# Kernel tuning notes

Measured on AMD Instinct MI355X. Metric: run time of the kernel, lower is better.

## Reference

```python
import jax, jax.numpy as jnp
import numpy as np

B, CIR_LEN, AUX_DIM, T, CD, DS, DCONV = 16, 16384, 14, 512, 256, 16, 4
SEG = CIR_LEN // T          # 32
DI = 2 * CD                 # d_inner = 512


def layer_norm(x, g, b, eps=1e-5):
    m = jnp.mean(x, -1, keepdims=True)
    v = jnp.var(x, -1, keepdims=True)
    return (x - m) * jax.lax.rsqrt(v + eps) * g + b


def gelu(x):
    return jax.nn.gelu(x, approximate=False)  # torch default exact GELU


def selective_ssm(x, in_proj_w, conv_w, conv_b, x_proj_w, dt_proj_w, dt_proj_b, A_log, D, out_proj_w):
    # x: (B, L, CD)
    Bsz, L, _ = x.shape
    xz = x @ in_proj_w.T                      # (B, L, 2*DI)
    x_in, z = jnp.split(xz, 2, axis=-1)       # each (B, L, DI)
    # depthwise causal conv (pad d_conv-1 left, truncate to L == torch pad both + [:L])
    xp = jnp.pad(x_in, ((0, 0), (DCONV - 1, 0), (0, 0)))
    x_conv = sum(xp[:, k:k + L, :] * conv_w[:, k] for k in range(DCONV)) + conv_b
    x_conv = jax.nn.silu(x_conv)              # (B, L, DI)
    ssm_in = x_conv @ x_proj_w.T              # (B, L, 1+2*DS)
    dt_raw = ssm_in[..., :1]
    B_ssm = ssm_in[..., 1:1 + DS]             # (B, L, DS)
    C_ssm = ssm_in[..., 1 + DS:]              # (B, L, DS)
    delta = jax.nn.softplus(dt_raw @ dt_proj_w.T + dt_proj_b)      # (B, L, DI)
    A = -jnp.exp(A_log)                                            # (DI, DS)
    deltaA = jnp.exp(delta[..., None] * A)                         # (B, L, DI, DS)
    deltaB_u = delta[..., None] * B_ssm[:, :, None, :] * x_conv[..., None]

    def step(h, inp):
        dA, dBu, c = inp
        h = dA * h + dBu                       # (B, DI, DS)
        y = jnp.einsum('bds,bs->bd', h, c)     # (B, DI)
        return h, y

    h0 = jnp.zeros((Bsz, DI, DS), x.dtype)
    _, ys = jax.lax.scan(step, h0, (jnp.moveaxis(deltaA, 1, 0),
                                    jnp.moveaxis(deltaB_u, 1, 0),
                                    jnp.moveaxis(C_ssm, 1, 0)))
    y = jnp.moveaxis(ys, 0, 1)                 # (B, L, DI)
    y = y + x_conv * D
    y = y * jax.nn.silu(z)
    return y @ out_proj_w.T                    # (B, L, CD)


def setup_inputs() -> dict:
    key = jax.random.key(0)
    ks = iter(jax.random.split(key, 32))
    rn = lambda shape, s=0.02: jax.random.normal(next(ks), shape, jnp.float32) * s
    return {
        'cir': jax.random.normal(next(ks), (B, CIR_LEN), jnp.float32),
        'aux': jax.random.normal(next(ks), (B, AUX_DIM), jnp.float32),
        'cir_proj_w': rn((CD, SEG)),
        'cir_norm_g': jnp.ones((CD,)), 'cir_norm_b': jnp.zeros((CD,)),
        'aux_proj_w': rn((CD, AUX_DIM)),
        'aux_norm_g': jnp.ones((CD,)), 'aux_norm_b': jnp.zeros((CD,)),
        'm_norm_g': jnp.ones((CD,)), 'm_norm_b': jnp.zeros((CD,)),
        'in_proj_w': rn((2 * DI, CD)),
        'conv_w': rn((DI, DCONV)), 'conv_b': jnp.zeros((DI,)),
        'x_proj_w': rn((1 + 2 * DS, DI)),
        'dt_proj_w': rn((DI, 1)), 'dt_proj_b': jnp.zeros((DI,)),
        'A_log': jnp.log(jnp.broadcast_to(jnp.arange(1, DS + 1, dtype=jnp.float32), (DI, DS))),
        'D': jnp.ones((DI,)),
        'out_proj_w': rn((CD, DI)),
        'mid_w': rn((CD, CD)), 'mid_b': jnp.zeros((CD,)),
        'mid_norm_g': jnp.ones((CD,)), 'mid_norm_b': jnp.zeros((CD,)),
        'bn_g': jnp.ones((CD,)), 'bn_b': jnp.zeros((CD,)),
        'fc1_w': rn((CD // 2, CD)), 'fc1_b': jnp.zeros((CD // 2,)),
        'fc2_w': rn((1, CD // 2)), 'fc2_b': jnp.zeros((1,)),
    }


def reference(cir, aux, cir_proj_w, cir_norm_g, cir_norm_b, aux_proj_w, aux_norm_g, aux_norm_b,
              m_norm_g, m_norm_b, in_proj_w, conv_w, conv_b, x_proj_w, dt_proj_w, dt_proj_b,
              A_log, D, out_proj_w, mid_w, mid_b, mid_norm_g, mid_norm_b, bn_g, bn_b,
              fc1_w, fc1_b, fc2_w, fc2_b):
    # eval mode: dropout = identity, BatchNorm uses running stats (mean 0, var 1)
    x_seg = cir.reshape(cir.shape[0], T, SEG)
    h_cir = gelu(layer_norm(x_seg @ cir_proj_w.T, cir_norm_g, cir_norm_b))
    h_aux = gelu(layer_norm(aux @ aux_proj_w.T, aux_norm_g, aux_norm_b))[:, None, :]
    h = h_cir + h_aux                          # (B, T, CD)
    h = h + selective_ssm(layer_norm(h, m_norm_g, m_norm_b), in_proj_w, conv_w, conv_b,
                          x_proj_w, dt_proj_w, dt_proj_b, A_log, D, out_proj_w)
    hp = jnp.mean(h, axis=1)                   # AdaptiveAvgPool1d(1)
    h2 = gelu(layer_norm(hp @ mid_w.T + mid_b, mid_norm_g, mid_norm_b))
    hbn = h2 * jax.lax.rsqrt(jnp.float32(1.0 + 1e-5)) * bn_g + bn_b
    h3 = gelu(hbn @ fc1_w.T + fc1_b)
    return (h3 @ fc2_w.T + fc2_b)[:, 0]
```

## Files before the change

kernel.cpp:

```cpp
#include <hip/hip_runtime.h>
#include <hip/hip_bf16.h>

typedef __hip_bfloat16 bf16;
typedef __attribute__((ext_vector_type(8))) short short8;
typedef __attribute__((ext_vector_type(4))) float f32x4;

#define Bsz   16
#define Tn    512
#define SEG   32
#define CD    256
#define DI    512
#define DS    16
#define DCONV 4
#define BT    (Bsz*Tn)
#define NPART 32

__device__ __forceinline__ float erf_fast(float x) {
  float ax = fabsf(x);
  float t = 1.0f / (1.0f + 0.3275911f * ax);
  float p = t * (0.254829592f + t * (-0.284496736f + t * (1.421413741f +
            t * (-1.453152027f + t * 1.061405429f))));
  float r = 1.0f - p * __expf(-ax * ax);
  return copysignf(r, x);
}
__device__ __forceinline__ float gelu_f(float x) {
  return 0.5f * x * (1.0f + erf_fast(x * 0.7071067811865476f));
}
__device__ __forceinline__ float silu_f(float x) {
  return x / (1.0f + __expf(-x));
}
__device__ __forceinline__ float softplus_f(float x) {
  return fmaxf(x, 0.0f) + __logf(1.0f + __expf(-fabsf(x)));
}
__device__ __forceinline__ float bfu(unsigned short u) {
  return __uint_as_float(((unsigned int)u) << 16);
}
__device__ __forceinline__ unsigned short f2bfu(float x) {
  bf16 h = __float2bfloat16(x);
  return *(unsigned short*)&h;
}
__device__ __forceinline__ float block_sum256(float v, float* red) {
  int tid = threadIdx.x;
  #pragma unroll
  for (int off = 32; off > 0; off >>= 1) v += __shfl_down(v, off, 64);
  __syncthreads();
  if ((tid & 63) == 0) red[tid >> 6] = v;
  __syncthreads();
  return red[0] + red[1] + red[2] + red[3];
}

__global__ __launch_bounds__(256) void prep_kernel(
    const float* __restrict__ aux, const float* __restrict__ apw,
    const float* __restrict__ g, const float* __restrict__ bb,
    const float* __restrict__ in_w, const float* __restrict__ xpw,
    const float* __restrict__ cpw,
    bf16* __restrict__ w_in, bf16* __restrict__ wpad, bf16* __restrict__ cpwT,
    float* __restrict__ haux)
{
  __shared__ float red[4];
  int i = blockIdx.x * 256 + threadIdx.x;
  if (i < 262144) {
    int e = i & 7, lane = (i >> 3) & 63, k0 = (i >> 9) & 7, nb = i >> 12;
    int fr = lane & 15, q = lane >> 4;
    w_in[i] = __float2bfloat16(in_w[(size_t)(nb * 16 + fr) * 256 + k0 * 32 + q * 8 + e]);
  } else if (i < 294912) {
    int o = i - 262144;
    int e = o & 7, lane = (o >> 3) & 63, k0 = (o >> 9) & 15, nb = o >> 13;
    int fr = lane & 15, q = lane >> 4;
    int row = nb * 16 + fr, k = k0 * 32 + q * 8 + e;
    float v = 0.f;
    if (row < 32)       v = xpw[(1 + row) * 512 + k];
    else if (row == 32) v = xpw[k];
    wpad[o] = __float2bfloat16(v);
  } else {
    int o = i - 294912;
    int k = o >> 8, j = o & 255;
    cpwT[o] = __float2bfloat16(cpw[j * 32 + k]);
  }
  if (blockIdx.x < 16) {
    int b = blockIdx.x, j = threadIdx.x;
    float acc = 0.f;
    #pragma unroll
    for (int k = 0; k < 14; ++k)
      acc += aux[b * 14 + k] * apw[j * 14 + k];
    float s1 = block_sum256(acc, red);
    float s2 = block_sum256(acc * acc, red);
    float mean = s1 * (1.f / 256.f);
    float var  = s2 * (1.f / 256.f) - mean * mean;
    float xn = (acc - mean) * rsqrtf(var + 1e-5f) * g[j] + bb[j];
    haux[b * 256 + j] = gelu_f(xn);
  }
}

__global__ __launch_bounds__(512) void row_inproj_kernel(
    const float* __restrict__ cir, const bf16* __restrict__ cpwT,
    const float* __restrict__ cg, const float* __restrict__ cb,
    const float* __restrict__ mg, const float* __restrict__ mb,
    const float* __restrict__ haux, const bf16* __restrict__ w_in,
    bf16* __restrict__ xzbf, float* __restrict__ hp_part)
{
  __shared__ float hps[8][256];
  __shared__ __align__(16) unsigned short xns[16][264];
  int tid = threadIdx.x;
  int wave = tid >> 6, lane = tid & 63;
  int r0 = blockIdx.x * 16 + wave * 2;
  int b = blockIdx.x >> 5;
  int j0 = lane * 4;

  float vj[2][4] = {};
  for (int c = 0; c < 8; ++c) {
    float xk[2][4];
    #pragma unroll
    for (int r4 = 0; r4 < 2; ++r4) {
      float4 xv = ((const float4*)(cir + (size_t)(r0 + r4) * SEG))[c];
      xk[r4][0] = xv.x; xk[r4][1] = xv.y; xk[r4][2] = xv.z; xk[r4][3] = xv.w;
    }
    #pragma unroll
    for (int kk = 0; kk < 4; ++kk) {
      int k = c * 4 + kk;
      uint2 wv = *(const uint2*)((const unsigned short*)cpwT + k * 256 + j0);
      float w0 = __uint_as_float(wv.x << 16);
      float w1 = __uint_as_float(wv.x & 0xffff0000u);
      float w2 = __uint_as_float(wv.y << 16);
      float w3 = __uint_as_float(wv.y & 0xffff0000u);
      #pragma unroll
      for (int r4 = 0; r4 < 2; ++r4) {
        float xv = xk[r4][kk];
        vj[r4][0] += xv * w0; vj[r4][1] += xv * w1;
        vj[r4][2] += xv * w2; vj[r4][3] += xv * w3;
      }
    }
  }
  float s[2], q2[2];
  #pragma unroll
  for (int r4 = 0; r4 < 2; ++r4) {
    s[r4]  = vj[r4][0] + vj[r4][1] + vj[r4][2] + vj[r4][3];
    q2[r4] = vj[r4][0]*vj[r4][0] + vj[r4][1]*vj[r4][1]
           + vj[r4][2]*vj[r4][2] + vj[r4][3]*vj[r4][3];
  }
  #pragma unroll
  for (int off = 32; off > 0; off >>= 1) {
    #pragma unroll
    for (int r4 = 0; r4 < 2; ++r4) {
      s[r4]  += __shfl_xor(s[r4],  off, 64);
      q2[r4] += __shfl_xor(q2[r4], off, 64);
    }
  }
  float4 cgv = *(const float4*)(cg + j0);
  float4 cbv = *(const float4*)(cb + j0);
  float4 hxv = *(const float4*)(haux + b * 256 + j0);
  float hv[2][4];
  float hs[2], hq[2];
  #pragma unroll
  for (int r4 = 0; r4 < 2; ++r4) {
    float mean = s[r4] * (1.f/256.f);
    float var  = q2[r4] * (1.f/256.f) - mean * mean;
    float inv  = rsqrtf(var + 1e-5f);
    float g0 = gelu_f((vj[r4][0] - mean) * inv * cgv.x + cbv.x) + hxv.x;
    float g1 = gelu_f((vj[r4][1] - mean) * inv * cgv.y + cbv.y) + hxv.y;
    float g2 = gelu_f((vj[r4][2] - mean) * inv * cgv.z + cbv.z) + hxv.z;
    float g3 = gelu_f((vj[r4][3] - mean) * inv * cgv.w + cbv.w) + hxv.w;
    hv[r4][0] = g0; hv[r4][1] = g1; hv[r4][2] = g2; hv[r4][3] = g3;
    hs[r4] = g0 + g1 + g2 + g3;
    hq[r4] = g0*g0 + g1*g1 + g2*g2 + g3*g3;
  }
  #pragma unroll
  for (int off = 32; off > 0; off >>= 1) {
    #pragma unroll
    for (int r4 = 0; r4 < 2; ++r4) {
      hs[r4] += __shfl_xor(hs[r4], off, 64);
      hq[r4] += __shfl_xor(hq[r4], off, 64);
    }
  }
  float4 mgv = *(const float4*)(mg + j0);
  float4 mbv = *(const float4*)(mb + j0);
  #pragma unroll
  for (int r4 = 0; r4 < 2; ++r4) {
    float m2  = hs[r4] * (1.f/256.f);
    float v2  = hq[r4] * (1.f/256.f) - m2 * m2;
    float inv2 = rsqrtf(v2 + 1e-5f);
    unsigned int lo = (unsigned int)f2bfu((hv[r4][0] - m2) * inv2 * mgv.x + mbv.x) |
                      ((unsigned int)f2bfu((hv[r4][1] - m2) * inv2 * mgv.y + mbv.y) << 16);
    unsigned int hi = (unsigned int)f2bfu((hv[r4][2] - m2) * inv2 * mgv.z + mbv.z) |
                      ((unsigned int)f2bfu((hv[r4][3] - m2) * inv2 * mgv.w + mbv.w) << 16);
    uint2 pk; pk.x = lo; pk.y = hi;
    *(uint2*)&xns[wave * 2 + r4][j0] = pk;
  }
  #pragma unroll
  for (int q = 0; q < 4; ++q)
    hps[wave][j0 + q] = hv[0][q] + hv[1][q];
  __syncthreads();
  if (tid < 256) {
    int j = tid;
    float part = hps[0][j] + hps[1][j] + hps[2][j] + hps[3][j]
               + hps[4][j] + hps[5][j] + hps[6][j] + hps[7][j];
    hp_part[(size_t)(blockIdx.x & (NPART - 1)) * 4096 + b * 256 + j] =
        part * (1.f / 512.f);
  }
  {
    int fr = lane & 15, quad = lane >> 4;
    int rbase = blockIdx.x * 16;
    const short* Wp = (const short*)w_in;
    unsigned short* xzp = (unsigned short*)xzbf;
    #pragma unroll
    for (int nt = 0; nt < 8; ++nt) {
      int nb = wave * 8 + nt;
      f32x4 acc = {0.f, 0.f, 0.f, 0.f};
      #pragma unroll
      for (int k0 = 0; k0 < 8; ++k0) {
        int ka = k0 * 32 + quad * 8;
        short8 a = *(const short8*)&xns[fr][ka];
        short8 bb8 = *(const short8*)(Wp + (((size_t)nb * 8 + k0) * 64 + lane) * 8);
        acc = __builtin_amdgcn_mfma_f32_16x16x32_bf16(a, bb8, acc, 0, 0, 0);
      }
      int n0 = nb * 16;
      int crow = quad * 4;
      #pragma unroll
      for (int i = 0; i < 4; ++i)
        xzp[(size_t)(rbase + crow + i) * 1024 + n0 + fr] = f2bfu(acc[i]);
    }
  }
}

__global__ __launch_bounds__(512) void conv_xproj_kernel(
    const bf16* __restrict__ xzbf, const bf16* __restrict__ wpad,
    const float* __restrict__ cw, const float* __restrict__ cbv,
    float* __restrict__ ssm)
{
  __shared__ __align__(16) unsigned short xst[35][512];
  __shared__ __align__(16) unsigned short xcs[32][520];
  int c = blockIdx.x, b = blockIdx.y;
  int t0 = c * 32;
  int tid = threadIdx.x;
  const unsigned short* xzp = (const unsigned short*)xzbf;

  for (int it = tid; it < 2240; it += 512) {
    int row = it >> 6, c8 = it & 63;
    int t = t0 - 3 + row;
    uint4 v = make_uint4(0u, 0u, 0u, 0u);
    if (t >= 0)
      v = *(const uint4*)(xzp + ((size_t)((b << 9) + t)) * 1024 + c8 * 8);
    *(uint4*)&xst[row][c8 * 8] = v;
  }
  __syncthreads();

  {
    int d = tid;
    float4 w = *(const float4*)(cw + d * 4);
    float cbd = cbv[d];
    float pa = bfu(xst[0][d]), pb = bfu(xst[1][d]), pc = bfu(xst[2][d]);
    #pragma unroll
    for (int i = 0; i < 32; ++i) {
      float x = bfu(xst[3 + i][d]);
      float a = cbd + w.x * pa + w.y * pb + w.z * pc + w.w * x;
      pa = pb; pb = pc; pc = x;
      xcs[i][d] = f2bfu(silu_f(a));
    }
  }
  __syncthreads();

  {
    int wave = tid >> 6, lane = tid & 63;
    int fr = lane & 15, quad = lane >> 4;
    int mh = wave >> 2;
    int nb = wave & 3;
    int n0 = nb * 16;
    f32x4 acc = {0.f, 0.f, 0.f, 0.f};
    const short* Wp = (const short*)wpad;
    #pragma unroll
    for (int k0 = 0; k0 < 16; ++k0) {
      int ka = k0 * 32 + quad * 8;
      short8 a = *(const short8*)&xcs[mh * 16 + fr][ka];
      short8 b8 = *(const short8*)(Wp + (((size_t)nb * 16 + k0) * 64 + lane) * 8);
      acc = __builtin_amdgcn_mfma_f32_16x16x32_bf16(a, b8, acc, 0, 0, 0);
    }
    int ccol = lane & 15, crow = quad * 4;
    #pragma unroll
    for (int i = 0; i < 4; ++i)
      ssm[((size_t)((b << 9) + t0 + mh * 16 + crow + i)) * 64 + n0 + ccol] = acc[i];
  }
}

__global__ __launch_bounds__(1024) void scan_full_kernel(
    const bf16* __restrict__ xzbf, const float* __restrict__ ssm,
    const float* __restrict__ cw, const float* __restrict__ cbv,
    const float* __restrict__ dtw, const float* __restrict__ dtb,
    const float* __restrict__ A_log, const float* __restrict__ Dd,
    float* __restrict__ ybar)
{
  __shared__ __align__(16) unsigned short xraw[2][35][32];
  __shared__ __align__(16) unsigned short zraw[2][32][32];
  __shared__ __align__(8)  float BC[2][32][34];
  __shared__ float dts[2][32];
  __shared__ __align__(16) float cgd[2][32][32][4];
  __shared__ float xdp_s[32][32];
  __shared__ float hendA[32][16];
  __shared__ float ybh[2][32];

  int dgrp = blockIdx.x, b = blockIdx.y;
  int tid = threadIdx.x;
  int d0 = dgrp * 32;
  int bb = b << 9;
  const unsigned short* xzp = (const unsigned short*)xzbf;

  int s  = tid & 15;
  int dp = (tid >> 4) & 31;
  int qh = tid >> 9;
  int dS = d0 + dp;
  float As  = -__expf(A_log[dS * 16 + s]);
  int d2 = tid & 31, r32 = (tid >> 5) & 31;
  int dC = d0 + d2;
  float4 wc = *(const float4*)(cw + dC * 4);
  float cbd = cbv[dC];
  float wdC = dtw[dC], bdC = dtb[dC];

  float h = 0.f, yacc = 0.f, P = 1.f, K = 0.f, xdp = 0.f;

  for (int p = 0; p < 8; ++p) {
    __syncthreads();
    if (tid < 512) {
      for (int it = tid; it < 536; it += 512) {
        int q = it >= 268;
        int e = it - (q ? 268 : 0);
        int t0q = q * 256 + p * 32;
        if (e < 140) {
          int row = e >> 2, c4 = e & 3;
          int t = t0q - 3 + row;
          uint4 v = make_uint4(0u, 0u, 0u, 0u);
          if (t >= 0)
            v = *(const uint4*)(xzp + (size_t)(bb + t) * 1024 + d0 + c4 * 8);
          *(uint4*)&xraw[q][row][c4 * 8] = v;
        } else {
          int e2 = e - 140;
          int row = e2 >> 2, c4 = e2 & 3;
          uint4 v = *(const uint4*)(xzp + (size_t)(bb + t0q + row) * 1024 + 512 + d0 + c4 * 8);
          *(uint4*)&zraw[q][row][c4 * 8] = v;
        }
      }
    } else {
      int t2 = tid - 512;
      int q = t2 >> 8;
      int r = (t2 >> 3) & 31, l8 = t2 & 7;
      int t0q = q * 256 + p * 32;
      const float* srow = ssm + (size_t)(bb + t0q + r) * 64;
      float4 v = *(const float4*)(srow + l8 * 4);
      int cc = l8 * 4;
      if (cc < 16) {
        BC[q][r][cc*2]   = v.x; BC[q][r][cc*2+2] = v.y;
        BC[q][r][cc*2+4] = v.z; BC[q][r][cc*2+6] = v.w;
      } else {
        int c2 = cc - 16;
        BC[q][r][c2*2+1] = v.x; BC[q][r][c2*2+3] = v.y;
        BC[q][r][c2*2+5] = v.z; BC[q][r][c2*2+7] = v.w;
      }
      if (l8 == 0) dts[q][r] = srow[32];
    }
    __syncthreads();
    #pragma unroll
    for (int q = 0; q < 2; ++q) {
      int ii = r32;
      float xa = bfu(xraw[q][ii][d2]);
      float xb = bfu(xraw[q][ii + 1][d2]);
      float xm = bfu(xraw[q][ii + 2][d2]);
      float xd = bfu(xraw[q][ii + 3][d2]);
      float a = cbd + wc.x * xa + wc.y * xb + wc.z * xm + wc.w * xd;
      float xc = bfu(f2bfu(silu_f(a)));
      float gt = silu_f(bfu(zraw[q][ii][d2]));
      float de = softplus_f(dts[q][ii] * wdC + bdC);
      xdp += xc * gt;
      float4 pk; pk.x = de * xc; pk.y = gt; pk.z = de; pk.w = 0.f;
      *(float4*)&cgd[q][ii][d2][0] = pk;
    }
    __syncthreads();
    #pragma unroll
    for (int i = 0; i < 32; ++i) {
      float4 cg = *(const float4*)&cgd[qh][i][dp][0];
      float2 bc = *(const float2*)&BC[qh][i][s * 2];
      float a = __expf(As * cg.z);
      h = a * h + cg.x * bc.x;
      float w = bc.y * cg.y;
      yacc += h * w;
      if (qh) { P *= a; K += P * w; }
    }
  }
  xdp_s[r32][d2] = xdp;
  if (qh == 0) hendA[dp][s] = h;
  __syncthreads();
  if (qh == 1) yacc += hendA[dp][s] * K;
  yacc += __shfl_xor(yacc, 1, 64);
  yacc += __shfl_xor(yacc, 2, 64);
  yacc += __shfl_xor(yacc, 4, 64);
  yacc += __shfl_xor(yacc, 8, 64);
  if (s == 0) ybh[qh][dp] = yacc;
  __syncthreads();
  if (qh == 0 && s == 0) {
    float xds = 0.f;
    #pragma unroll
    for (int k = 0; k < 32; ++k) xds += xdp_s[k][dp];
    ybar[b * 512 + dS] = ybh[0][dp] + ybh[1][dp] + Dd[dS] * xds;
  }
}

__global__ __launch_bounds__(256) void head_kernel(
    const float* __restrict__ hp_part, const float* __restrict__ ybar,
    const float* __restrict__ w_out,
    const float* __restrict__ midw, const float* __restrict__ midb,
    const float* __restrict__ mng, const float* __restrict__ mnb,
    const float* __restrict__ bng, const float* __restrict__ bnb,
    const float* __restrict__ f1w, const float* __restrict__ f1b,
    const float* __restrict__ f2w, const float* __restrict__ f2b,
    float* __restrict__ out)
{
  __shared__ float red[4];
  __shared__ __align__(16) float yb[512];
  __shared__ __align__(16) float shp[256];
  __shared__ __align__(16) float sh[256];
  __shared__ __align__(16) float sh2[128];
  int b = blockIdx.x, j = threadIdx.x;
  yb[j]       = ybar[b * 512 + j];
  yb[256 + j] = ybar[b * 512 + 256 + j];
  float hv = 0.f;
  #pragma unroll
  for (int p = 0; p < NPART; ++p)
    hv += hp_part[(size_t)p * 4096 + b * 256 + j];
  __syncthreads();
  {
    float acc2 = 0.f;
    const float4* wr = (const float4*)(w_out + j * 512);
    const float4* yv = (const float4*)yb;
    #pragma unroll 4
    for (int k = 0; k < 128; ++k) {
      float4 w = wr[k], x = yv[k];
      acc2 += w.x * x.x + w.y * x.y + w.z * x.z + w.w * x.w;
    }
    hv += acc2 * (1.f / 512.f);
  }
  shp[j] = hv;
  __syncthreads();
  float acc = midb[j];
  {
    const float4* mw = (const float4*)(midw + j * 256);
    const float4* sv = (const float4*)shp;
    #pragma unroll 4
    for (int k = 0; k < 64; ++k) {
      float4 w = mw[k], xv = sv[k];
      acc += w.x * xv.x + w.y * xv.y + w.z * xv.z + w.w * xv.w;
    }
  }
  float s1 = block_sum256(acc, red);
  float s2 = block_sum256(acc * acc, red);
  float mean = s1 * (1.f / 256.f);
  float var  = s2 * (1.f / 256.f) - mean * mean;
  float h2 = gelu_f((acc - mean) * rsqrtf(var + 1e-5f) * mng[j] + mnb[j]);
  float hbn = h2 * rsqrtf(1.0f + 1e-5f) * bng[j] + bnb[j];
  sh[j] = hbn;
  __syncthreads();
  if (j < 128) {
    float a2 = f1b[j];
    const float4* fw = (const float4*)(f1w + j * 256);
    const float4* sv = (const float4*)sh;
    #pragma unroll 4
    for (int k = 0; k < 64; ++k) {
      float4 w = fw[k], xv = sv[k];
      a2 += w.x * xv.x + w.y * xv.y + w.z * xv.z + w.w * xv.w;
    }
    sh2[j] = gelu_f(a2);
  }
  __syncthreads();
  if (j == 0) {
    float o = f2b[0];
    const float4* fw = (const float4*)f2w;
    const float4* sv = (const float4*)sh2;
    for (int k = 0; k < 32; ++k) {
      float4 w = fw[k], xv = sv[k];
      o += w.x * xv.x + w.y * xv.y + w.z * xv.z + w.w * xv.w;
    }
    out[b] = o;
  }
}

extern "C" void kernel_launch(void* const* d_in, const int* in_sizes, int n_in,
                              void* d_out, int out_size, void* d_ws, size_t ws_size,
                              hipStream_t stream)
{
  const float* cir        = (const float*)d_in[0];
  const float* aux        = (const float*)d_in[1];
  const float* cir_proj_w = (const float*)d_in[2];
  const float* cir_norm_g = (const float*)d_in[3];
  const float* cir_norm_b = (const float*)d_in[4];
  const float* aux_proj_w = (const float*)d_in[5];
  const float* aux_norm_g = (const float*)d_in[6];
  const float* aux_norm_b = (const float*)d_in[7];
  const float* m_norm_g   = (const float*)d_in[8];
  const float* m_norm_b   = (const float*)d_in[9];
  const float* in_proj_w  = (const float*)d_in[10];
  const float* conv_w     = (const float*)d_in[11];
  const float* conv_b     = (const float*)d_in[12];
  const float* x_proj_w   = (const float*)d_in[13];
  const float* dt_proj_w  = (const float*)d_in[14];
  const float* dt_proj_b  = (const float*)d_in[15];
  const float* A_log      = (const float*)d_in[16];
  const float* Dd         = (const float*)d_in[17];
  const float* out_proj_w = (const float*)d_in[18];
  const float* mid_w      = (const float*)d_in[19];
  const float* mid_b      = (const float*)d_in[20];
  const float* mid_norm_g = (const float*)d_in[21];
  const float* mid_norm_b = (const float*)d_in[22];
  const float* bn_g       = (const float*)d_in[23];
  const float* bn_b       = (const float*)d_in[24];
  const float* fc1_w      = (const float*)d_in[25];
  const float* fc1_b      = (const float*)d_in[26];
  const float* fc2_w      = (const float*)d_in[27];
  const float* fc2_b      = (const float*)d_in[28];
  float* out = (float*)d_out;

  float* ws      = (float*)d_ws;
  bf16*  xzbf    = (bf16*)ws;
  float* ssm     = ws + 4194304;
  bf16*  w_inbf  = (bf16*)(ssm + 524288);
  bf16*  wpadbf  = (bf16*)((float*)w_inbf + 131072);
  bf16*  cpwTbf  = (bf16*)((float*)wpadbf + 16384);
  float* haux    = (float*)cpwTbf + 4096;
  float* hp_part = haux + 4096;
  float* ybar    = hp_part + 131072;

  prep_kernel<<<1184, 256, 0, stream>>>(aux, aux_proj_w, aux_norm_g, aux_norm_b,
                                        in_proj_w, x_proj_w, cir_proj_w,
                                        w_inbf, wpadbf, cpwTbf, haux);
  row_inproj_kernel<<<512, 512, 0, stream>>>(cir, cpwTbf, cir_norm_g, cir_norm_b,
                                             m_norm_g, m_norm_b, haux, w_inbf,
                                             xzbf, hp_part);
  conv_xproj_kernel<<<dim3(16, Bsz), 512, 0, stream>>>(xzbf, wpadbf, conv_w, conv_b,
                                                       ssm);
  scan_full_kernel<<<dim3(16, Bsz), 1024, 0, stream>>>(xzbf, ssm, conv_w, conv_b,
                                                       dt_proj_w, dt_proj_b,
                                                       A_log, Dd, ybar);
  head_kernel<<<16, 256, 0, stream>>>(hp_part, ybar, out_proj_w,
                                      mid_w, mid_b, mid_norm_g, mid_norm_b,
                                      bn_g, bn_b, fc1_w, fc1_b, fc2_w, fc2_b, out);
}
```

Baseline: 215.0 us.

## Store z and conv output in per-channel-group transposed layout; reuse conv result in scan

The in-projection now writes x and z to separate buffers, with z laid out per batch and 32-channel group so each time step is a contiguous 64-byte row. The conv kernel also writes its SiLU conv output in the same transposed layout, so the scan reads ready conv values instead of recomputing the depthwise conv and SiLU. This removes redundant conv math and the strided 64-byte gathers from 2KB-stride rows in the scan's loads. The cost is an extra global write of the conv output and scattered 2-byte stores for z in the in-projection epilogue.

Measured after the change: 217.6 us. No clear change (+1.2%).

```diff
diff --git a/kernel.cpp b/kernel.cpp
--- a/kernel.cpp
+++ b/kernel.cpp
@@ -97,7 +97,8 @@
     const float* __restrict__ cg, const float* __restrict__ cb,
     const float* __restrict__ mg, const float* __restrict__ mb,
     const float* __restrict__ haux, const bf16* __restrict__ w_in,
-    bf16* __restrict__ xzbf, float* __restrict__ hp_part)
+    bf16* __restrict__ xbf, bf16* __restrict__ zTg,
+    float* __restrict__ hp_part)
 {
   __shared__ float hps[8][256];
   __shared__ __align__(16) unsigned short xns[16][264];
@@ -200,8 +201,10 @@
   {
     int fr = lane & 15, quad = lane >> 4;
     int rbase = blockIdx.x * 16;
+    int tl0 = (blockIdx.x & 31) * 16 + quad * 4;
     const short* Wp = (const short*)w_in;
-    unsigned short* xzp = (unsigned short*)xzbf;
+    unsigned short* xp = (unsigned short*)xbf;
+    unsigned short* zp = (unsigned short*)zTg;
     #pragma unroll
     for (int nt = 0; nt < 8; ++nt) {
       int nb = wave * 8 + nt;
@@ -213,33 +216,41 @@
         short8 bb8 = *(const short8*)(Wp + (((size_t)nb * 8 + k0) * 64 + lane) * 8);
         acc = __builtin_amdgcn_mfma_f32_16x16x32_bf16(a, bb8, acc, 0, 0, 0);
       }
-      int n0 = nb * 16;
+      int n = nb * 16 + fr;
       int crow = quad * 4;
-      #pragma unroll
-      for (int i = 0; i < 4; ++i)
-        xzp[(size_t)(rbase + crow + i) * 1024 + n0 + fr] = f2bfu(acc[i]);
+      if (nb < 32) {
+        #pragma unroll
+        for (int i = 0; i < 4; ++i)
+          xp[(size_t)(rbase + crow + i) * 512 + n] = f2bfu(acc[i]);
+      } else {
+        int d = n - 512, dg = d >> 5, d2 = d & 31;
+        size_t base = ((size_t)(b * 16 + dg) * 512 + tl0) * 32 + d2;
+        #pragma unroll
+        for (int i = 0; i < 4; ++i)
+          zp[base + (size_t)i * 32] = f2bfu(acc[i]);
+      }
     }
   }
 }
 
 __global__ __launch_bounds__(512) void conv_xproj_kernel(
-    const bf16* __restrict__ xzbf, const bf16* __restrict__ wpad,
+    const bf16* __restrict__ xbf, const bf16* __restrict__ wpad,
     const float* __restrict__ cw, const float* __restrict__ cbv,
-    float* __restrict__ ssm)
+    float* __restrict__ ssm, bf16* __restrict__ xcT)
 {
   __shared__ __align__(16) unsigned short xst[35][512];
   __shared__ __align__(16) unsigned short xcs[32][520];
   int c = blockIdx.x, b = blockIdx.y;
   int t0 = c * 32;
   int tid = threadIdx.x;
-  const unsigned short* xzp = (const unsigned short*)xzbf;
+  const unsigned short* xzp = (const unsigned short*)xbf;
 
   for (int it = tid; it < 2240; it += 512) {
     int row = it >> 6, c8 = it & 63;
     int t = t0 - 3 + row;
     uint4 v = make_uint4(0u, 0u, 0u, 0u);
     if (t >= 0)
-      v = *(const uint4*)(xzp + ((size_t)((b << 9) + t)) * 1024 + c8 * 8);
+      v = *(const uint4*)(xzp + ((size_t)((b << 9) + t)) * 512 + c8 * 8);
     *(uint4*)&xst[row][c8 * 8] = v;
   }
   __syncthreads();
@@ -258,6 +269,14 @@
     }
   }
   __syncthreads();
+
+  {
+    int dg = tid >> 5, tl = tid & 31;
+    uint4* dst = (uint4*)((unsigned short*)xcT +
+                          (((size_t)(b * 16 + dg)) * 512 + t0 + tl) * 32);
+    const uint4* src = (const uint4*)&xcs[tl][dg * 32];
+    dst[0] = src[0]; dst[1] = src[1]; dst[2] = src[2]; dst[3] = src[3];
+  }
 
   {
     int wave = tid >> 6, lane = tid & 63;
@@ -282,14 +301,14 @@
 }
 
 __global__ __launch_bounds__(1024) void scan_full_kernel(
-    const bf16* __restrict__ xzbf, const float* __restrict__ ssm,
-    const float* __restrict__ cw, const float* __restrict__ cbv,
+    const bf16* __restrict__ xcT, const bf16* __restrict__ zTg,
+    const float* __restrict__ ssm,
     const float* __restrict__ dtw, const float* __restrict__ dtb,
     const float* __restrict__ A_log, const float* __restrict__ Dd,
     float* __restrict__ ybar)
 {
-  __shared__ __align__(16) unsigned short xraw[2][35][32];
-  __shared__ __align__(16) unsigned short zraw[2][32][32];
+  __shared__ __align__(16) unsigned short xct[2][32][32];
+  __shared__ __align__(16) unsigned short zt[2][32][32];
   __shared__ __align__(8)  float BC[2][32][34];
   __shared__ float dts[2][32];
   __shared__ __align__(16) float cgd[2][32][32][4];
@@ -299,19 +318,16 @@
 
   int dgrp = blockIdx.x, b = blockIdx.y;
   int tid = threadIdx.x;
-  int d0 = dgrp * 32;
   int bb = b << 9;
-  const unsigned short* xzp = (const unsigned short*)xzbf;
+  size_t trow = ((size_t)(b * 16 + dgrp)) * 512;
 
   int s  = tid & 15;
   int dp = (tid >> 4) & 31;
   int qh = tid >> 9;
-  int dS = d0 + dp;
+  int dS = dgrp * 32 + dp;
   float As  = -__expf(A_log[dS * 16 + s]);
   int d2 = tid & 31, r32 = (tid >> 5) & 31;
-  int dC = d0 + d2;
-  float4 wc = *(const float4*)(cw + dC * 4);
-  float cbd = cbv[dC];
+  int dC = dgrp * 32 + d2;
   float wdC = dtw[dC], bdC = dtb[dC];
 
   float h = 0.f, yacc = 0.f, P = 1.f, K = 0.f, xdp = 0.f;
@@ -319,24 +335,15 @@
   for (int p = 0; p < 8; ++p) {
     __syncthreads();
     if (tid < 512) {
-      for (int it = tid; it < 536; it += 512) {
-        int q = it >= 268;
-        int e = it - (q ? 268 : 0);
-        int t0q = q * 256 + p * 32;
-        if (e < 140) {
-          int row = e >> 2, c4 = e & 3;
-          int t = t0q - 3 + row;
-          uint4 v = make_uint4(0u, 0u, 0u, 0u);
-          if (t >= 0)
-            v = *(const uint4*)(xzp + (size_t)(bb + t) * 1024 + d0 + c4 * 8);
-          *(uint4*)&xraw[q][row][c4 * 8] = v;
-        } else {
-          int e2 = e - 140;
-          int row = e2 >> 2, c4 = e2 & 3;
-          uint4 v = *(const uint4*)(xzp + (size_t)(bb + t0q + row) * 1024 + 512 + d0 + c4 * 8);
-          *(uint4*)&zraw[q][row][c4 * 8] = v;
-        }
-      }
+      int kind = tid >> 8;
+      int q = (tid >> 7) & 1;
+      int e = tid & 127;
+      int row = e >> 2, c4 = e & 3;
+      int t = q * 256 + p * 32 + row;
+      const unsigned short* src = (const unsigned short*)(kind ? zTg : xcT);
+      uint4 v = *(const uint4*)(src + (trow + t) * 32 + c4 * 8);
+      if (kind) *(uint4*)&zt[q][row][c4 * 8] = v;
+      else      *(uint4*)&xct[q][row][c4 * 8] = v;
     } else {
       int t2 = tid - 512;
       int q = t2 >> 8;
@@ -358,18 +365,12 @@
     __syncthreads();
     #pragma unroll
     for (int q = 0; q < 2; ++q) {
-      int ii = r32;
-      float xa = bfu(xraw[q][ii][d2]);
-      float xb = bfu(xraw[q][ii + 1][d2]);
-      float xm = bfu(xraw[q][ii + 2][d2]);
-      float xd = bfu(xraw[q][ii + 3][d2]);
-      float a = cbd + wc.x * xa + wc.y * xb + wc.z * xm + wc.w * xd;
-      float xc = bfu(f2bfu(silu_f(a)));
-      float gt = silu_f(bfu(zraw[q][ii][d2]));
-      float de = softplus_f(dts[q][ii] * wdC + bdC);
+      float xc = bfu(xct[q][r32][d2]);
+      float gt = silu_f(bfu(zt[q][r32][d2]));
+      float de = softplus_f(dts[q][r32] * wdC + bdC);
       xdp += xc * gt;
       float4 pk; pk.x = de * xc; pk.y = gt; pk.z = de; pk.w = 0.f;
-      *(float4*)&cgd[q][ii][d2][0] = pk;
+      *(float4*)&cgd[q][r32][d2][0] = pk;
     }
     __syncthreads();
     #pragma unroll
@@ -515,8 +516,10 @@
   float* out = (float*)d_out;
 
   float* ws      = (float*)d_ws;
-  bf16*  xzbf    = (bf16*)ws;
-  float* ssm     = ws + 4194304;
+  bf16*  xbf     = (bf16*)ws;
+  bf16*  zTg     = (bf16*)(ws + 2097152);
+  bf16*  xcT     = (bf16*)(ws + 4194304);
+  float* ssm     = ws + 6291456;
   bf16*  w_inbf  = (bf16*)(ssm + 524288);
   bf16*  wpadbf  = (bf16*)((float*)w_inbf + 131072);
   bf16*  cpwTbf  = (bf16*)((float*)wpadbf + 16384);
@@ -529,10 +532,10 @@
                                         w_inbf, wpadbf, cpwTbf, haux);
   row_inproj_kernel<<<512, 512, 0, stream>>>(cir, cpwTbf, cir_norm_g, cir_norm_b,
                                              m_norm_g, m_norm_b, haux, w_inbf,
-                                             xzbf, hp_part);
-  conv_xproj_kernel<<<dim3(16, Bsz), 512, 0, stream>>>(xzbf, wpadbf, conv_w, conv_b,
-                                                       ssm);
-  scan_full_kernel<<<dim3(16, Bsz), 1024, 0, stream>>>(xzbf, ssm, conv_w, conv_b,
+                                             xbf, zTg, hp_part);
+  conv_xproj_kernel<<<dim3(16, Bsz), 512, 0, stream>>>(xbf, wpadbf, conv_w, conv_b,
+                                                       ssm, xcT);
+  scan_full_kernel<<<dim3(16, Bsz), 1024, 0, stream>>>(xcT, zTg, ssm,
                                                        dt_proj_w, dt_proj_b,
                                                        A_log, Dd, ybar);
   head_kernel<<<16, 256, 0, stream>>>(hp_part, ybar, out_proj_w,
```
